# Kernel optimization log

Measured on AMD Instinct MI355X. Metric: run time of the kernel, lower is better.

## Reference

```python
import jax, jax.numpy as jnp
import numpy as np

# Config matching init_kwargs: kernel_size=1, patch_size=21, stride=1,
# padding=0, dilation=1, dilation_patch=2  -> patch-based branch.
PATCH = 21
DIL_P = 2
STRIDE = 1
HALF = PATCH // 2          # 10
PAD = HALF * DIL_P         # 20


def setup_inputs() -> dict:
    key = jax.random.key(0)
    k1, k2 = jax.random.split(key)
    B, C, H, W = 8, 256, 96, 96
    input1 = jax.random.normal(k1, (B, C, H, W), dtype=jnp.float32)
    input2 = jax.random.normal(k2, (B, C, H, W), dtype=jnp.float32)
    return {"input1": input1, "input2": input2}


def reference(input1, input2):
    # Faithful to the torch module's _correlation_patch_based: both inputs are
    # sampled at the SAME shifted location, so
    #   out[b, ph, pw, y, x] = sum_c in1[b,c,y',x'] * in2[b,c,y',x']
    # with y' = y*stride + (ph-HALF)*DIL_P (zero if out of bounds).
    B, C, H, W = input1.shape
    out_h = (H - 1) // STRIDE + 1
    out_w = (W - 1) // STRIDE + 1

    # Per-pixel dot product over channels: [B, H, W]
    D = jnp.sum(input1 * input2, axis=1)
    # Zero-pad so out-of-bounds shifts read zeros
    Dp = jnp.pad(D, ((0, 0), (PAD, PAD), (PAD, PAD)))

    shifts = (jnp.arange(PATCH) - HALF) * DIL_P            # [P]
    ys = jnp.arange(out_h) * STRIDE                        # [oh]
    xs = jnp.arange(out_w) * STRIDE                        # [ow]
    yi = shifts[:, None] + ys[None, :] + PAD               # [P, oh]
    xi = shifts[:, None] + xs[None, :] + PAD               # [P, ow]

    # Gather: [B, P, P, oh, ow]
    out = Dp[:, yi[:, None, :, None], xi[None, :, None, :]]
    return out.reshape(B, PATCH * PATCH, out_h, out_w)
```

## Files before the change

### kernel.cpp

```cpp
#include <hip/hip_runtime.h>

constexpr int B = 8, C = 256, H = 96, W = 96;
constexpr int HW = H * W;
constexpr int NPIX = B * HW;
constexpr int PATCH = 21;
constexpr int HALF = PATCH / 2;
constexpr int DIL = 2;
constexpr int P2 = PATCH * PATCH;

__global__ __launch_bounds__(256) void dot_kernel(const float* __restrict__ a,
                                                  const float* __restrict__ b,
                                                  float* __restrict__ D) {
    int pix = blockIdx.x * blockDim.x + threadIdx.x;
    if (pix >= NPIX) return;
    int bb = pix / HW;
    int hw = pix - bb * HW;
    const float* pa = a + (size_t)bb * C * HW + hw;
    const float* pb = b + (size_t)bb * C * HW + hw;
    float acc0 = 0.f, acc1 = 0.f, acc2 = 0.f, acc3 = 0.f;
    #pragma unroll 4
    for (int c = 0; c < C; c += 4) {
        float a0 = pa[(size_t)(c + 0) * HW];
        float a1 = pa[(size_t)(c + 1) * HW];
        float a2 = pa[(size_t)(c + 2) * HW];
        float a3 = pa[(size_t)(c + 3) * HW];
        float b0 = pb[(size_t)(c + 0) * HW];
        float b1 = pb[(size_t)(c + 1) * HW];
        float b2 = pb[(size_t)(c + 2) * HW];
        float b3 = pb[(size_t)(c + 3) * HW];
        acc0 = fmaf(a0, b0, acc0);
        acc1 = fmaf(a1, b1, acc1);
        acc2 = fmaf(a2, b2, acc2);
        acc3 = fmaf(a3, b3, acc3);
    }
    D[pix] = (acc0 + acc1) + (acc2 + acc3);
}

__global__ __launch_bounds__(256) void scatter_kernel(const float* __restrict__ D,
                                                      float* __restrict__ out) {
    constexpr int W4 = W / 4;
    constexpr int TOTAL = B * P2 * H * W4;
    int tid = blockIdx.x * blockDim.x + threadIdx.x;
    if (tid >= TOTAL) return;

    int x4 = tid % W4;
    int t  = tid / W4;
    int y  = t % H;  t /= H;
    int p  = t % P2; t /= P2;
    int bb = t;

    int py = p / PATCH;
    int px = p - py * PATCH;
    int sy = y + (py - HALF) * DIL;
    int x0 = x4 * 4;
    int sx0 = x0 + (px - HALF) * DIL;

    float4 v = make_float4(0.f, 0.f, 0.f, 0.f);
    if (sy >= 0 && sy < H) {
        const float* row = D + (size_t)(bb * H + sy) * W;
        if (sx0 >= 0 && sx0 + 3 < W) {
            float2 lo = *(const float2*)(row + sx0);
            float2 hi = *(const float2*)(row + sx0 + 2);
            v = make_float4(lo.x, lo.y, hi.x, hi.y);
        } else {
            float* pv = &v.x;
            #pragma unroll
            for (int i = 0; i < 4; ++i) {
                int sx = sx0 + i;
                if (sx >= 0 && sx < W) pv[i] = row[sx];
            }
        }
    }
    reinterpret_cast<float4*>(out)[tid] = v;
}

extern "C" void kernel_launch(void* const* d_in, const int* in_sizes, int n_in,
                              void* d_out, int out_size, void* d_ws, size_t ws_size,
                              hipStream_t stream) {
    const float* in1 = (const float*)d_in[0];
    const float* in2 = (const float*)d_in[1];
    float* out = (float*)d_out;
    float* D = (float*)d_ws;

    {
        int threads = 256;
        int blocks = (NPIX + threads - 1) / threads;
        dot_kernel<<<blocks, threads, 0, stream>>>(in1, in2, D);
    }
    {
        constexpr int TOTAL = B * P2 * H * (W / 4);
        int threads = 256;
        int blocks = (TOTAL + threads - 1) / threads;
        scatter_kernel<<<blocks, threads, 0, stream>>>(D, out);
    }
}
```

Baseline: 244.4 us.

## Split channel reduction across wavefronts and use 3D grid for scatter

The dot kernel now assigns each 256-thread block a 64-pixel chunk. Its four wavefronts each reduce a quarter of the channels, and the partial sums are combined through shared memory. This gives each thread a shorter serial load chain and puts more independent memory streams in flight per pixel. The scatter kernel switches to a 3D grid (pixel-tile, patch offset, batch), which removes most of the integer div/mod index decoding and uses unsigned bounds checks. In exchange, the dot kernel pays for a shared-memory reduction and a block barrier, and fewer threads write results.

```diff
diff --git a/kernel.cpp b/kernel.cpp
--- a/kernel.cpp
+++ b/kernel.cpp
@@ -8,56 +8,66 @@
 constexpr int DIL = 2;
 constexpr int P2 = PATCH * PATCH;
 
+constexpr int CHUNKS_PER_B = HW / 64;
+
 __global__ __launch_bounds__(256) void dot_kernel(const float* __restrict__ a,
                                                   const float* __restrict__ b,
                                                   float* __restrict__ D) {
-    int pix = blockIdx.x * blockDim.x + threadIdx.x;
-    if (pix >= NPIX) return;
-    int bb = pix / HW;
-    int hw = pix - bb * HW;
-    const float* pa = a + (size_t)bb * C * HW + hw;
-    const float* pb = b + (size_t)bb * C * HW + hw;
-    float acc0 = 0.f, acc1 = 0.f, acc2 = 0.f, acc3 = 0.f;
+    __shared__ float red[256];
+    const int l = threadIdx.x & 63;
+    const int w = threadIdx.x >> 6;
+    const int blk = blockIdx.x;
+    const int bb = blk / CHUNKS_PER_B;
+    const int chunk = blk - bb * CHUNKS_PER_B;
+    const int hw = chunk * 64 + l;
+
+    const float* pa = a + ((size_t)bb * C + (size_t)w * 64) * HW + hw;
+    const float* pb = b + ((size_t)bb * C + (size_t)w * 64) * HW + hw;
+
+    float s0 = 0.f, s1 = 0.f, s2 = 0.f, s3 = 0.f;
     #pragma unroll 4
-    for (int c = 0; c < C; c += 4) {
-        float a0 = pa[(size_t)(c + 0) * HW];
-        float a1 = pa[(size_t)(c + 1) * HW];
-        float a2 = pa[(size_t)(c + 2) * HW];
-        float a3 = pa[(size_t)(c + 3) * HW];
-        float b0 = pb[(size_t)(c + 0) * HW];
-        float b1 = pb[(size_t)(c + 1) * HW];
-        float b2 = pb[(size_t)(c + 2) * HW];
-        float b3 = pb[(size_t)(c + 3) * HW];
-        acc0 = fmaf(a0, b0, acc0);
-        acc1 = fmaf(a1, b1, acc1);
-        acc2 = fmaf(a2, b2, acc2);
-        acc3 = fmaf(a3, b3, acc3);
+    for (int c = 0; c < 64; c += 4) {
+        float a0 = pa[0];
+        float a1 = pa[(size_t)HW];
+        float a2 = pa[(size_t)2 * HW];
+        float a3 = pa[(size_t)3 * HW];
+        float b0 = pb[0];
+        float b1 = pb[(size_t)HW];
+        float b2 = pb[(size_t)2 * HW];
+        float b3 = pb[(size_t)3 * HW];
+        pa += (size_t)4 * HW;
+        pb += (size_t)4 * HW;
+        s0 = fmaf(a0, b0, s0);
+        s1 = fmaf(a1, b1, s1);
+        s2 = fmaf(a2, b2, s2);
+        s3 = fmaf(a3, b3, s3);
     }
-    D[pix] = (acc0 + acc1) + (acc2 + acc3);
+
+    red[threadIdx.x] = (s0 + s1) + (s2 + s3);
+    __syncthreads();
+    if (w == 0) {
+        float r = (red[l] + red[l + 64]) + (red[l + 128] + red[l + 192]);
+        D[(size_t)bb * HW + hw] = r;
+    }
 }
 
 __global__ __launch_bounds__(256) void scatter_kernel(const float* __restrict__ D,
                                                       float* __restrict__ out) {
     constexpr int W4 = W / 4;
-    constexpr int TOTAL = B * P2 * H * W4;
-    int tid = blockIdx.x * blockDim.x + threadIdx.x;
-    if (tid >= TOTAL) return;
+    const int t = blockIdx.x * 256 + threadIdx.x;
+    const int y  = t / W4;
+    const int x4 = t - y * W4;
+    const int p  = blockIdx.y;
+    const int bb = blockIdx.z;
 
-    int x4 = tid % W4;
-    int t  = tid / W4;
-    int y  = t % H;  t /= H;
-    int p  = t % P2; t /= P2;
-    int bb = t;
-
-    int py = p / PATCH;
-    int px = p - py * PATCH;
-    int sy = y + (py - HALF) * DIL;
-    int x0 = x4 * 4;
-    int sx0 = x0 + (px - HALF) * DIL;
+    const int py = p / PATCH;
+    const int px = p - py * PATCH;
+    const int sy  = y + (py - HALF) * DIL;
+    const int sx0 = x4 * 4 + (px - HALF) * DIL;
 
     float4 v = make_float4(0.f, 0.f, 0.f, 0.f);
-    if (sy >= 0 && sy < H) {
-        const float* row = D + (size_t)(bb * H + sy) * W;
+    if ((unsigned)sy < (unsigned)H) {
+        const float* row = D + ((size_t)bb * H + sy) * W;
         if (sx0 >= 0 && sx0 + 3 < W) {
             float2 lo = *(const float2*)(row + sx0);
             float2 hi = *(const float2*)(row + sx0 + 2);
@@ -67,11 +77,13 @@
             #pragma unroll
             for (int i = 0; i < 4; ++i) {
                 int sx = sx0 + i;
-                if (sx >= 0 && sx < W) pv[i] = row[sx];
+                if ((unsigned)sx < (unsigned)W) pv[i] = row[sx];
             }
         }
     }
-    reinterpret_cast<float4*>(out)[tid] = v;
+
+    const size_t o = (size_t)(bb * P2 + p) * (H * W4) + t;
+    reinterpret_cast<float4*>(out)[o] = v;
 }
 
 extern "C" void kernel_launch(void* const* d_in, const int* in_sizes, int n_in,
@@ -83,14 +95,9 @@
     float* D = (float*)d_ws;
 
     {
-        int threads = 256;
-        int blocks = (NPIX + threads - 1) / threads;
-        dot_kernel<<<blocks, threads, 0, stream>>>(in1, in2, D);
+        dot_kernel<<<B * CHUNKS_PER_B, 256, 0, stream>>>(in1, in2, D);
     }
     {
-        constexpr int TOTAL = B * P2 * H * (W / 4);
-        int threads = 256;
-        int blocks = (TOTAL + threads - 1) / threads;
-        scatter_kernel<<<blocks, threads, 0, stream>>>(D, out);
+        scatter_kernel<<<dim3((H * (W / 4)) / 256, P2, B), 256, 0, stream>>>(D, out);
     }
 }
```

Result: no change. 244.2 us (-0.1%).
